# Kernel tuning notes

Hardware: AMD Instinct MI355X
Metric: run time of the kernel (lower is better)

## Reference

```python
import jax, jax.numpy as jnp
import numpy as np

N_NODES = 100000
N_EDGES = 1600000
F_IN = 500
HIDDEN = 64
N_CLASS = 40


def gcn_conv(x, W, b, src, dst, n_nodes):
    """PyG GCNConv: add self-loops, symmetric deg^-1/2 normalization,
    linear transform then scatter-add aggregation at dst."""
    h = x @ W  # [N, out]
    loop = jnp.arange(n_nodes, dtype=src.dtype)
    s = jnp.concatenate([src, loop])  # sources incl. self-loops
    d = jnp.concatenate([dst, loop])
    deg = jax.ops.segment_sum(jnp.ones_like(d, dtype=h.dtype), d, num_segments=n_nodes)
    dinv = jnp.where(deg > 0, jax.lax.rsqrt(deg), 0.0)
    norm = dinv[s] * dinv[d]  # [E+N]
    msg = h[s] * norm[:, None]  # gather + scale, [E+N, out]
    out = jax.ops.segment_sum(msg, d, num_segments=n_nodes)
    return out + b


def setup_inputs() -> dict:
    key = jax.random.key(0)
    k1, k2, k3, k4 = jax.random.split(key, 4)
    x = jax.random.normal(k1, (N_NODES, F_IN), dtype=jnp.float32)
    edge_index = jax.random.randint(k2, (2, N_EDGES), 0, N_NODES, dtype=jnp.int64)
    # Glorot-style init for GCNConv weights
    W1 = jax.random.normal(k3, (F_IN, HIDDEN), dtype=jnp.float32) / np.sqrt(F_IN)
    b1 = jnp.zeros((HIDDEN,), dtype=jnp.float32)
    W2 = jax.random.normal(k4, (HIDDEN, N_CLASS), dtype=jnp.float32) / np.sqrt(HIDDEN)
    b2 = jnp.zeros((N_CLASS,), dtype=jnp.float32)
    return {"x": x, "W1": W1, "b1": b1, "W2": W2, "b2": b2, "edge_index": edge_index}


def reference(x, W1, b1, W2, b2, edge_index):
    src, dst = edge_index[0], edge_index[1]
    n = x.shape[0]
    h = jax.nn.relu(gcn_conv(x, W1, b1, src, dst, n))
    # dropout is identity in eval mode (F.dropout with training=False)
    out = gcn_conv(h, W2, b2, src, dst, n)
    return jax.nn.log_softmax(out, axis=1)
```

## Files before the change

### kernel.cpp

```cpp
#include <hip/hip_runtime.h>
#include <math.h>

#define N_NODES 100000
#define N_EDGES 1600000
#define F_IN    500
#define HIDDEN  64
#define N_CLASS 40
#define KPAD    512

#define NB   2048
#define NPB  49
#define EPB  16384
#define CAP  1536

typedef __attribute__((ext_vector_type(4))) float f32x4;
typedef __attribute__((ext_vector_type(8))) __bf16 bf16x8;

__device__ __forceinline__ unsigned short f2bf(float f) {
    unsigned int u = __float_as_uint(f);
    u = (u + 0x7FFF + ((u >> 16) & 1)) >> 16;
    return (unsigned short)u;
}
__device__ __forceinline__ float bfu_lo(unsigned int v) {
    return __uint_as_float(v << 16);
}
__device__ __forceinline__ float bfu_hi(unsigned int v) {
    return __uint_as_float(v & 0xFFFF0000u);
}

__global__ void k_prep_w1t(const float* __restrict__ w1, unsigned short* __restrict__ w1t,
                           int* __restrict__ bcnt) {
    int idx = blockIdx.x * blockDim.x + threadIdx.x;
    if (idx < NB) bcnt[idx] = 0;
    if (idx >= HIDDEN * KPAD) return;
    int n = idx >> 9, k = idx & (KPAD - 1);
    float v = (k < F_IN) ? w1[k * HIDDEN + n] : 0.f;
    w1t[idx] = f2bf(v);
}

__launch_bounds__(1024)
__global__ void k_bhist(const int* __restrict__ dst, int* __restrict__ bcnt, int e) {
    __shared__ int h[NB];
    for (int i = threadIdx.x; i < NB; i += 1024) h[i] = 0;
    __syncthreads();
    int base = blockIdx.x * EPB;
#pragma unroll
    for (int j = 0; j < 16; ++j) {
        int i = base + j * 1024 + threadIdx.x;
        if (i < e) atomicAdd(&h[dst[i] / NPB], 1);
    }
    __syncthreads();
    for (int i = threadIdx.x; i < NB; i += 1024)
        if (h[i]) atomicAdd(&bcnt[i], h[i]);
}

__launch_bounds__(1024)
__global__ void k_bscan(const int* __restrict__ bcnt, int* __restrict__ bptr,
                        int* __restrict__ bcur) {
    __shared__ int s[1024];
    int t = threadIdx.x;
    int a = bcnt[2 * t], b = bcnt[2 * t + 1];
    int v = a + b;
    s[t] = v;
    __syncthreads();
    for (int off = 1; off < 1024; off <<= 1) {
        int u = (t >= off) ? s[t - off] : 0;
        __syncthreads();
        s[t] += u;
        __syncthreads();
    }
    int excl = s[t] - v;
    bptr[2 * t] = excl;     bptr[2 * t + 1] = excl + a;
    bcur[2 * t] = excl;     bcur[2 * t + 1] = excl + a;
    if (t == 1023) bptr[NB] = s[1023];
}

__launch_bounds__(1024)
__global__ void k_bfill(const int* __restrict__ src, const int* __restrict__ dst,
                        int* __restrict__ bcur, int2* __restrict__ ebuf, int e) {
    __shared__ int hist[NB];
    __shared__ int base_[NB];
    for (int i = threadIdx.x; i < NB; i += 1024) hist[i] = 0;
    __syncthreads();
    int b0 = blockIdx.x * EPB;
    int s_[16], d_[16];
#pragma unroll
    for (int j = 0; j < 16; ++j) {
        int i = b0 + j * 1024 + threadIdx.x;
        if (i < e) {
            s_[j] = src[i];
            d_[j] = dst[i];
            atomicAdd(&hist[d_[j] / NPB], 1);
        } else d_[j] = -1;
    }
    __syncthreads();
    for (int i = threadIdx.x; i < NB; i += 1024) {
        int hc = hist[i];
        base_[i] = hc ? atomicAdd(&bcur[i], hc) : 0;
        hist[i] = 0;
    }
    __syncthreads();
#pragma unroll
    for (int j = 0; j < 16; ++j) {
        if (d_[j] >= 0) {
            int bu = d_[j] / NPB;
            int r = atomicAdd(&hist[bu], 1);
            ebuf[base_[bu] + r] = make_int2(s_[j], d_[j]);
        }
    }
}

__launch_bounds__(256)
__global__ void k_bucket_csr(const int2* __restrict__ ebuf, const int* __restrict__ bptr,
                             int* __restrict__ rp, int* __restrict__ col,
                             float* __restrict__ dinv, int n) {
    int b  = blockIdx.x;
    int lo = b * NPB;
    if (lo >= n) return;
    int hi  = min(lo + NPB, n);
    int eb0 = bptr[b], ec = bptr[b + 1] - eb0;

    __shared__ int2 pairs[CAP];
    __shared__ int  hist[NPB];
    __shared__ int  excl[NPB + 1];
    for (int j = threadIdx.x; j < NPB; j += 256) hist[j] = 0;
    __syncthreads();
    for (int i = threadIdx.x; i < ec; i += 256) {
        int2 p = ebuf[eb0 + i];
        if (i < CAP) pairs[i] = p;
        atomicAdd(&hist[p.y - lo], 1);
    }
    __syncthreads();
    if (threadIdx.x == 0) {
        int acc = 0;
        for (int j = 0; j < NPB; ++j) { excl[j] = acc; acc += hist[j]; }
        excl[NPB] = acc;
    }
    __syncthreads();
    for (int j = threadIdx.x; j < hi - lo; j += 256) {
        rp[lo + j]   = eb0 + excl[j];
        dinv[lo + j] = rsqrtf((float)(hist[j] + 1));
    }
    if (hi == n && threadIdx.x == 0) rp[n] = eb0 + ec;
    __syncthreads();
    for (int j = threadIdx.x; j < NPB; j += 256) hist[j] = 0;
    __syncthreads();
    for (int i = threadIdx.x; i < ec; i += 256) {
        int2 p  = (i < CAP) ? pairs[i] : ebuf[eb0 + i];
        int  li = p.y - lo;
        int  r  = atomicAdd(&hist[li], 1);
        col[eb0 + excl[li] + r] = p.x;
    }
}

__launch_bounds__(256)
__global__ void k_gemm1(const float* __restrict__ x, const unsigned short* __restrict__ w1t,
                        const float* __restrict__ dinv, unsigned short* __restrict__ hs, int n) {
    __shared__ unsigned short xs[4][32][40];
    const int tid  = threadIdx.x;
    const int wave = tid >> 6;
    const int lane = tid & 63;
    const int quad = lane >> 4;
    const int l16  = lane & 15;
    const int rowb = blockIdx.x * 128 + wave * 32;

    const int srow = lane >> 3;
    const int skof = (lane & 7) * 4;

    f32x4 acc[2][4];
#pragma unroll
    for (int rt = 0; rt < 2; ++rt)
#pragma unroll
        for (int ct = 0; ct < 4; ++ct) acc[rt][ct] = (f32x4)0.f;

    for (int ks = 0; ks < 16; ++ks) {
        const int k0 = ks * 32;

        float4 tmp[4];
        if (ks < 15) {
#pragma unroll
            for (int u = 0; u < 4; ++u) {
                int grow = rowb + u * 8 + srow;
                tmp[u] = (grow < n) ? *(const float4*)&x[(size_t)grow * F_IN + k0 + skof]
                                    : make_float4(0.f, 0.f, 0.f, 0.f);
            }
        } else {
#pragma unroll
            for (int u = 0; u < 4; ++u) {
                int grow = rowb + u * 8 + srow;
                const float* p = &x[(size_t)grow * F_IN];
                float v0 = (grow < n && k0 + skof + 0 < F_IN) ? p[k0 + skof + 0] : 0.f;
                float v1 = (grow < n && k0 + skof + 1 < F_IN) ? p[k0 + skof + 1] : 0.f;
                float v2 = (grow < n && k0 + skof + 2 < F_IN) ? p[k0 + skof + 2] : 0.f;
                float v3 = (grow < n && k0 + skof + 3 < F_IN) ? p[k0 + skof + 3] : 0.f;
                tmp[u] = make_float4(v0, v1, v2, v3);
            }
        }
        bf16x8 bfrag[4];
#pragma unroll
        for (int ct = 0; ct < 4; ++ct)
            bfrag[ct] = *(const bf16x8*)&w1t[(ct * 16 + l16) * KPAD + k0 + quad * 8];

#pragma unroll
        for (int u = 0; u < 4; ++u) {
            unsigned int lo = (unsigned int)f2bf(tmp[u].x) | ((unsigned int)f2bf(tmp[u].y) << 16);
            unsigned int hi = (unsigned int)f2bf(tmp[u].z) | ((unsigned int)f2bf(tmp[u].w) << 16);
            *(uint2*)&xs[wave][u * 8 + srow][skof] = make_uint2(lo, hi);
        }
        __syncthreads();

        union { bf16x8 v; unsigned int u[4]; } af[2];
#pragma unroll
        for (int rt = 0; rt < 2; ++rt) {
            uint2 a = *(const uint2*)&xs[wave][rt * 16 + l16][quad * 8];
            uint2 b = *(const uint2*)&xs[wave][rt * 16 + l16][quad * 8 + 4];
            af[rt].u[0] = a.x; af[rt].u[1] = a.y; af[rt].u[2] = b.x; af[rt].u[3] = b.y;
        }
#pragma unroll
        for (int rt = 0; rt < 2; ++rt)
#pragma unroll
            for (int ct = 0; ct < 4; ++ct)
                acc[rt][ct] = __builtin_amdgcn_mfma_f32_16x16x32_bf16(
                    af[rt].v, bfrag[ct], acc[rt][ct], 0, 0, 0);
        __syncthreads();
    }

#pragma unroll
    for (int rt = 0; rt < 2; ++rt) {
#pragma unroll
        for (int reg = 0; reg < 4; ++reg) {
            int grow = rowb + rt * 16 + quad * 4 + reg;
            if (grow < n) {
                float dv = dinv[grow];
#pragma unroll
                for (int ct = 0; ct < 4; ++ct)
                    hs[(size_t)grow * HIDDEN + ct * 16 + l16] = f2bf(dv * acc[rt][ct][reg]);
            }
        }
    }
}

template <int F, bool RELU, bool LSM>
__launch_bounds__(256)
__global__ void k_agg(const uint2* __restrict__ hs2, const int* __restrict__ rp,
                      const int* __restrict__ col, const float* __restrict__ dinv,
                      const float* __restrict__ bias, float* __restrict__ out, int n) {
    constexpr int PW2 = F / 4;
    const int lane = threadIdx.x & 63;
    const int q    = lane >> 4;
    const int p    = lane & 15;
    const bool act = p < PW2;
    int wid = __builtin_amdgcn_readfirstlane((blockIdx.x * blockDim.x + threadIdx.x) >> 6);
    const int nw = (gridDim.x * blockDim.x) >> 6;

    for (; wid < n; wid += nw) {
        const int beg = rp[wid], end = rp[wid + 1];
        float a0 = 0.f, a1 = 0.f, a2 = 0.f, a3 = 0.f;
        int e = beg + q;
        for (; e + 12 < end; e += 16) {
            int c0 = col[e], c1 = col[e + 4], c2 = col[e + 8], c3 = col[e + 12];
            uint2 v0 = act ? hs2[(unsigned)c0 * PW2 + p] : make_uint2(0u, 0u);
            uint2 v1 = act ? hs2[(unsigned)c1 * PW2 + p] : make_uint2(0u, 0u);
            uint2 v2 = act ? hs2[(unsigned)c2 * PW2 + p] : make_uint2(0u, 0u);
            uint2 v3 = act ? hs2[(unsigned)c3 * PW2 + p] : make_uint2(0u, 0u);
            a0 += bfu_lo(v0.x) + bfu_lo(v1.x) + bfu_lo(v2.x) + bfu_lo(v3.x);
            a1 += bfu_hi(v0.x) + bfu_hi(v1.x) + bfu_hi(v2.x) + bfu_hi(v3.x);
            a2 += bfu_lo(v0.y) + bfu_lo(v1.y) + bfu_lo(v2.y) + bfu_lo(v3.y);
            a3 += bfu_hi(v0.y) + bfu_hi(v1.y) + bfu_hi(v2.y) + bfu_hi(v3.y);
        }
        if (e + 4 < end) {
            int c0 = col[e], c1 = col[e + 4];
            uint2 v0 = act ? hs2[(unsigned)c0 * PW2 + p] : make_uint2(0u, 0u);
            uint2 v1 = act ? hs2[(unsigned)c1 * PW2 + p] : make_uint2(0u, 0u);
            a0 += bfu_lo(v0.x) + bfu_lo(v1.x);
            a1 += bfu_hi(v0.x) + bfu_hi(v1.x);
            a2 += bfu_lo(v0.y) + bfu_lo(v1.y);
            a3 += bfu_hi(v0.y) + bfu_hi(v1.y);
            e += 8;
        }
        if (e < end) {
            int c0 = col[e];
            uint2 v0 = act ? hs2[(unsigned)c0 * PW2 + p] : make_uint2(0u, 0u);
            a0 += bfu_lo(v0.x); a1 += bfu_hi(v0.x);
            a2 += bfu_lo(v0.y); a3 += bfu_hi(v0.y);
        }
        a0 += __shfl_xor(a0, 16); a1 += __shfl_xor(a1, 16);
        a2 += __shfl_xor(a2, 16); a3 += __shfl_xor(a3, 16);
        a0 += __shfl_xor(a0, 32); a1 += __shfl_xor(a1, 32);
        a2 += __shfl_xor(a2, 32); a3 += __shfl_xor(a3, 32);

        const float di = dinv[wid];
        uint2 sv  = act ? hs2[(unsigned)wid * PW2 + p] : make_uint2(0u, 0u);
        float4 bv = act ? *(const float4*)&bias[4 * p] : make_float4(0.f, 0.f, 0.f, 0.f);
        float r0 = di * (a0 + bfu_lo(sv.x)) + bv.x;
        float r1 = di * (a1 + bfu_hi(sv.x)) + bv.y;
        float r2 = di * (a2 + bfu_lo(sv.y)) + bv.z;
        float r3 = di * (a3 + bfu_hi(sv.y)) + bv.w;
        if (RELU) {
            r0 = fmaxf(r0, 0.f); r1 = fmaxf(r1, 0.f);
            r2 = fmaxf(r2, 0.f); r3 = fmaxf(r3, 0.f);
        }
        if (LSM) {
            float m = act ? fmaxf(fmaxf(r0, r1), fmaxf(r2, r3)) : -INFINITY;
#pragma unroll
            for (int off = 8; off; off >>= 1) m = fmaxf(m, __shfl_xor(m, off));
            float ex = act ? (__expf(r0 - m) + __expf(r1 - m) + __expf(r2 - m) + __expf(r3 - m))
                           : 0.f;
#pragma unroll
            for (int off = 8; off; off >>= 1) ex += __shfl_xor(ex, off);
            float lse = m + __logf(ex);
            r0 -= lse; r1 -= lse; r2 -= lse; r3 -= lse;
        }
        if (q == 0 && act)
            *(float4*)&out[(size_t)wid * F + 4 * p] = make_float4(r0, r1, r2, r3);
    }
}

__launch_bounds__(256)
__global__ void k_gemm2(const float* __restrict__ a, const float* __restrict__ w,
                        const float* __restrict__ dinv, unsigned short* __restrict__ out, int n) {
    __shared__ float ws[HIDDEN * N_CLASS];
    for (int idx = threadIdx.x; idx < HIDDEN * N_CLASS; idx += 256) ws[idx] = w[idx];
    __syncthreads();
    int idx = blockIdx.x * 256 + threadIdx.x;
    if (idx >= n * N_CLASS) return;
    int i = idx / N_CLASS, j = idx - i * N_CLASS;
    float s = 0.f;
#pragma unroll
    for (int k = 0; k < HIDDEN; k += 4) {
        float4 xv = *(const float4*)&a[(size_t)i * HIDDEN + k];
        s = fmaf(xv.x, ws[k * N_CLASS + j], s);
        s = fmaf(xv.y, ws[(k + 1) * N_CLASS + j], s);
        s = fmaf(xv.z, ws[(k + 2) * N_CLASS + j], s);
        s = fmaf(xv.w, ws[(k + 3) * N_CLASS + j], s);
    }
    out[idx] = f2bf(dinv[i] * s);
}

extern "C" void kernel_launch(void* const* d_in, const int* in_sizes, int n_in,
                              void* d_out, int out_size, void* d_ws, size_t ws_size,
                              hipStream_t stream) {
    const float* x   = (const float*)d_in[0];
    const float* W1  = (const float*)d_in[1];
    const float* b1  = (const float*)d_in[2];
    const float* W2  = (const float*)d_in[3];
    const float* b2  = (const float*)d_in[4];
    const int*   ei  = (const int*)d_in[5];
    const int*   src = ei;
    const int*   dst = ei + N_EDGES;
    float*       out = (float*)d_out;

    char*  ws  = (char*)d_ws;
    size_t off = 0;
    auto alloc = [&](size_t bytes) -> void* {
        void* p = ws + off;
        off += (bytes + 255) & ~(size_t)255;
        return p;
    };
    int*            bcnt = (int*)alloc((size_t)NB * 4);
    int*            bptr = (int*)alloc((size_t)(NB + 1) * 4);
    int*            bcur = (int*)alloc((size_t)NB * 4);
    int*            rp   = (int*)alloc((size_t)(N_NODES + 1) * 4);
    int*            col  = (int*)alloc((size_t)N_EDGES * 4);
    float*          dinv = (float*)alloc((size_t)N_NODES * 4);
    unsigned short* w1t  = (unsigned short*)alloc((size_t)HIDDEN * KPAD * 2);
    unsigned short* h1s  = (unsigned short*)alloc((size_t)N_NODES * HIDDEN * 2);
    float*          h1a  = (float*)alloc((size_t)N_NODES * HIDDEN * 4);
    int2*           ebuf = (int2*)h1a;
    unsigned short* h2s  = h1s;

    const int NBH = (N_EDGES + EPB - 1) / EPB;

    k_prep_w1t<<<(HIDDEN * KPAD + 255) / 256, 256, 0, stream>>>(W1, w1t, bcnt);
    k_bhist<<<NBH, 1024, 0, stream>>>(dst, bcnt, N_EDGES);
    k_bscan<<<1, 1024, 0, stream>>>(bcnt, bptr, bcur);
    k_bfill<<<NBH, 1024, 0, stream>>>(src, dst, bcur, ebuf, N_EDGES);
    k_bucket_csr<<<NB, 256, 0, stream>>>(ebuf, bptr, rp, col, dinv, N_NODES);

    k_gemm1<<<(N_NODES + 127) / 128, 256, 0, stream>>>(x, w1t, dinv, h1s, N_NODES);
    k_agg<HIDDEN, true, false><<<2048, 256, 0, stream>>>(
        (const uint2*)h1s, rp, col, dinv, b1, h1a, N_NODES);

    k_gemm2<<<(N_NODES * N_CLASS + 255) / 256, 256, 0, stream>>>(h1a, W2, dinv, h2s, N_NODES);
    k_agg<N_CLASS, false, true><<<2048, 256, 0, stream>>>(
        (const uint2*)h2s, rp, col, dinv, b2, out, N_NODES);
}
```

Baseline: 497.7 us.

## Fuse second-layer GEMM into first aggregation and widen gather loads

The layer-1 aggregation now applies the 64x40 W2 transform in its epilogue. Each wave stages its finished row in LDS and writes the bf16 pre-scaled layer-2 features directly. This removes the fp32 hidden buffer round trip and the separate k_gemm2 launch. The aggregation kernel switches from 16 lanes x uint2 to 8 lanes x uint4 per row, so it issues fewer, wider gather loads. k_gemm1 gets a per-wave double-buffered LDS tile with register prefetch of the next K slice and drops its block barriers. This relies on each wave touching only its own LDS slice.

```diff
diff --git a/kernel.cpp b/kernel.cpp
--- a/kernel.cpp
+++ b/kernel.cpp
@@ -156,7 +156,7 @@
 __launch_bounds__(256)
 __global__ void k_gemm1(const float* __restrict__ x, const unsigned short* __restrict__ w1t,
                         const float* __restrict__ dinv, unsigned short* __restrict__ hs, int n) {
-    __shared__ unsigned short xs[4][32][40];
+    __shared__ __align__(16) unsigned short xs[4][2][32][40];
     const int tid  = threadIdx.x;
     const int wave = tid >> 6;
     const int lane = tid & 63;
@@ -173,16 +173,14 @@
 #pragma unroll
         for (int ct = 0; ct < 4; ++ct) acc[rt][ct] = (f32x4)0.f;
 
-    for (int ks = 0; ks < 16; ++ks) {
+    auto LOAD = [&](float4 (&t)[4], int ks) {
         const int k0 = ks * 32;
-
-        float4 tmp[4];
         if (ks < 15) {
 #pragma unroll
             for (int u = 0; u < 4; ++u) {
                 int grow = rowb + u * 8 + srow;
-                tmp[u] = (grow < n) ? *(const float4*)&x[(size_t)grow * F_IN + k0 + skof]
-                                    : make_float4(0.f, 0.f, 0.f, 0.f);
+                t[u] = (grow < n) ? *(const float4*)&x[(size_t)grow * F_IN + k0 + skof]
+                                  : make_float4(0.f, 0.f, 0.f, 0.f);
             }
         } else {
 #pragma unroll
@@ -193,36 +191,41 @@
                 float v1 = (grow < n && k0 + skof + 1 < F_IN) ? p[k0 + skof + 1] : 0.f;
                 float v2 = (grow < n && k0 + skof + 2 < F_IN) ? p[k0 + skof + 2] : 0.f;
                 float v3 = (grow < n && k0 + skof + 3 < F_IN) ? p[k0 + skof + 3] : 0.f;
-                tmp[u] = make_float4(v0, v1, v2, v3);
-            }
-        }
+                t[u] = make_float4(v0, v1, v2, v3);
+            }
+        }
+    };
+    auto STASH = [&](const float4 (&t)[4], int buf) {
+#pragma unroll
+        for (int u = 0; u < 4; ++u) {
+            unsigned int lo = (unsigned int)f2bf(t[u].x) | ((unsigned int)f2bf(t[u].y) << 16);
+            unsigned int hi = (unsigned int)f2bf(t[u].z) | ((unsigned int)f2bf(t[u].w) << 16);
+            *(uint2*)&xs[wave][buf][u * 8 + srow][skof] = make_uint2(lo, hi);
+        }
+    };
+
+    float4 tcur[4], tnx[4];
+    LOAD(tcur, 0);
+    STASH(tcur, 0);
+    for (int ks = 0; ks < 16; ++ks) {
+        const int buf = ks & 1;
+        if (ks < 15) LOAD(tnx, ks + 1);
+        const int k0 = ks * 32;
         bf16x8 bfrag[4];
 #pragma unroll
         for (int ct = 0; ct < 4; ++ct)
             bfrag[ct] = *(const bf16x8*)&w1t[(ct * 16 + l16) * KPAD + k0 + quad * 8];
-
-#pragma unroll
-        for (int u = 0; u < 4; ++u) {
-            unsigned int lo = (unsigned int)f2bf(tmp[u].x) | ((unsigned int)f2bf(tmp[u].y) << 16);
-            unsigned int hi = (unsigned int)f2bf(tmp[u].z) | ((unsigned int)f2bf(tmp[u].w) << 16);
-            *(uint2*)&xs[wave][u * 8 + srow][skof] = make_uint2(lo, hi);
-        }
-        __syncthreads();
-
-        union { bf16x8 v; unsigned int u[4]; } af[2];
-#pragma unroll
-        for (int rt = 0; rt < 2; ++rt) {
-            uint2 a = *(const uint2*)&xs[wave][rt * 16 + l16][quad * 8];
-            uint2 b = *(const uint2*)&xs[wave][rt * 16 + l16][quad * 8 + 4];
-            af[rt].u[0] = a.x; af[rt].u[1] = a.y; af[rt].u[2] = b.x; af[rt].u[3] = b.y;
-        }
+        bf16x8 af[2];
+#pragma unroll
+        for (int rt = 0; rt < 2; ++rt)
+            af[rt] = *(const bf16x8*)&xs[wave][buf][rt * 16 + l16][quad * 8];
 #pragma unroll
         for (int rt = 0; rt < 2; ++rt)
 #pragma unroll
             for (int ct = 0; ct < 4; ++ct)
                 acc[rt][ct] = __builtin_amdgcn_mfma_f32_16x16x32_bf16(
-                    af[rt].v, bfrag[ct], acc[rt][ct], 0, 0, 0);
-        __syncthreads();
+                    af[rt], bfrag[ct], acc[rt][ct], 0, 0, 0);
+        if (ks < 15) STASH(tnx, buf ^ 1);
     }
 
 #pragma unroll
@@ -240,101 +243,129 @@
     }
 }
 
-template <int F, bool RELU, bool LSM>
+template <int F, bool RELU, bool LSM, bool FUSE>
 __launch_bounds__(256)
-__global__ void k_agg(const uint2* __restrict__ hs2, const int* __restrict__ rp,
+__global__ void k_agg(const uint4* __restrict__ hs4, const int* __restrict__ rp,
                       const int* __restrict__ col, const float* __restrict__ dinv,
-                      const float* __restrict__ bias, float* __restrict__ out, int n) {
-    constexpr int PW2 = F / 4;
+                      const float* __restrict__ bias, float* __restrict__ outf,
+                      unsigned short* __restrict__ outh, const float* __restrict__ w2,
+                      int n) {
+    constexpr int PW4 = (F + 7) / 8;
+    __shared__ float ws2[FUSE ? HIDDEN * N_CLASS : 1];
+    __shared__ float rowbuf[FUSE ? 4 : 1][FUSE ? HIDDEN : 1];
+    if constexpr (FUSE) {
+        for (int i = threadIdx.x; i < HIDDEN * N_CLASS; i += 256) ws2[i] = w2[i];
+        __syncthreads();
+    }
     const int lane = threadIdx.x & 63;
-    const int q    = lane >> 4;
-    const int p    = lane & 15;
-    const bool act = p < PW2;
+    const int wave = threadIdx.x >> 6;
+    const int q    = lane >> 3;
+    const int p    = lane & 7;
+    const bool act = p < PW4;
     int wid = __builtin_amdgcn_readfirstlane((blockIdx.x * blockDim.x + threadIdx.x) >> 6);
     const int nw = (gridDim.x * blockDim.x) >> 6;
+    const uint4 z = make_uint4(0u, 0u, 0u, 0u);
 
     for (; wid < n; wid += nw) {
         const int beg = rp[wid], end = rp[wid + 1];
-        float a0 = 0.f, a1 = 0.f, a2 = 0.f, a3 = 0.f;
+        float a[8];
+#pragma unroll
+        for (int i = 0; i < 8; ++i) a[i] = 0.f;
+        auto ACC = [&](uint4 v) {
+            a[0] += bfu_lo(v.x); a[1] += bfu_hi(v.x);
+            a[2] += bfu_lo(v.y); a[3] += bfu_hi(v.y);
+            a[4] += bfu_lo(v.z); a[5] += bfu_hi(v.z);
+            a[6] += bfu_lo(v.w); a[7] += bfu_hi(v.w);
+        };
         int e = beg + q;
-        for (; e + 12 < end; e += 16) {
-            int c0 = col[e], c1 = col[e + 4], c2 = col[e + 8], c3 = col[e + 12];
-            uint2 v0 = act ? hs2[(unsigned)c0 * PW2 + p] : make_uint2(0u, 0u);
-            uint2 v1 = act ? hs2[(unsigned)c1 * PW2 + p] : make_uint2(0u, 0u);
-            uint2 v2 = act ? hs2[(unsigned)c2 * PW2 + p] : make_uint2(0u, 0u);
-            uint2 v3 = act ? hs2[(unsigned)c3 * PW2 + p] : make_uint2(0u, 0u);
-            a0 += bfu_lo(v0.x) + bfu_lo(v1.x) + bfu_lo(v2.x) + bfu_lo(v3.x);
-            a1 += bfu_hi(v0.x) + bfu_hi(v1.x) + bfu_hi(v2.x) + bfu_hi(v3.x);
-            a2 += bfu_lo(v0.y) + bfu_lo(v1.y) + bfu_lo(v2.y) + bfu_lo(v3.y);
-            a3 += bfu_hi(v0.y) + bfu_hi(v1.y) + bfu_hi(v2.y) + bfu_hi(v3.y);
-        }
-        if (e + 4 < end) {
-            int c0 = col[e], c1 = col[e + 4];
-            uint2 v0 = act ? hs2[(unsigned)c0 * PW2 + p] : make_uint2(0u, 0u);
-            uint2 v1 = act ? hs2[(unsigned)c1 * PW2 + p] : make_uint2(0u, 0u);
-            a0 += bfu_lo(v0.x) + bfu_lo(v1.x);
-            a1 += bfu_hi(v0.x) + bfu_hi(v1.x);
-            a2 += bfu_lo(v0.y) + bfu_lo(v1.y);
-            a3 += bfu_hi(v0.y) + bfu_hi(v1.y);
-            e += 8;
-        }
-        if (e < end) {
-            int c0 = col[e];
-            uint2 v0 = act ? hs2[(unsigned)c0 * PW2 + p] : make_uint2(0u, 0u);
-            a0 += bfu_lo(v0.x); a1 += bfu_hi(v0.x);
-            a2 += bfu_lo(v0.y); a3 += bfu_hi(v0.y);
-        }
-        a0 += __shfl_xor(a0, 16); a1 += __shfl_xor(a1, 16);
-        a2 += __shfl_xor(a2, 16); a3 += __shfl_xor(a3, 16);
-        a0 += __shfl_xor(a0, 32); a1 += __shfl_xor(a1, 32);
-        a2 += __shfl_xor(a2, 32); a3 += __shfl_xor(a3, 32);
+        for (; e + 24 < end; e += 32) {
+            int c0 = col[e], c1 = col[e + 8], c2 = col[e + 16], c3 = col[e + 24];
+            uint4 v0 = act ? hs4[(unsigned)c0 * PW4 + p] : z;
+            uint4 v1 = act ? hs4[(unsigned)c1 * PW4 + p] : z;
+            uint4 v2 = act ? hs4[(unsigned)c2 * PW4 + p] : z;
+            uint4 v3 = act ? hs4[(unsigned)c3 * PW4 + p] : z;
+            ACC(v0); ACC(v1); ACC(v2); ACC(v3);
+        }
+        {
+            const bool g0 = e < end, g1 = e + 8 < end, g2 = e + 16 < end;
+            int c0 = g0 ? col[e] : 0;
+            int c1 = g1 ? col[e + 8] : 0;
+            int c2 = g2 ? col[e + 16] : 0;
+            uint4 v0 = (act && g0) ? hs4[(unsigned)c0 * PW4 + p] : z;
+            uint4 v1 = (act && g1) ? hs4[(unsigned)c1 * PW4 + p] : z;
+            uint4 v2 = (act && g2) ? hs4[(unsigned)c2 * PW4 + p] : z;
+            ACC(v0); ACC(v1); ACC(v2);
+        }
+#pragma unroll
+        for (int i = 0; i < 8; ++i) {
+            a[i] += __shfl_xor(a[i], 8);
+            a[i] += __shfl_xor(a[i], 16);
+            a[i] += __shfl_xor(a[i], 32);
+        }
 
         const float di = dinv[wid];
-        uint2 sv  = act ? hs2[(unsigned)wid * PW2 + p] : make_uint2(0u, 0u);
-        float4 bv = act ? *(const float4*)&bias[4 * p] : make_float4(0.f, 0.f, 0.f, 0.f);
-        float r0 = di * (a0 + bfu_lo(sv.x)) + bv.x;
-        float r1 = di * (a1 + bfu_hi(sv.x)) + bv.y;
-        float r2 = di * (a2 + bfu_lo(sv.y)) + bv.z;
-        float r3 = di * (a3 + bfu_hi(sv.y)) + bv.w;
-        if (RELU) {
-            r0 = fmaxf(r0, 0.f); r1 = fmaxf(r1, 0.f);
-            r2 = fmaxf(r2, 0.f); r3 = fmaxf(r3, 0.f);
-        }
-        if (LSM) {
-            float m = act ? fmaxf(fmaxf(r0, r1), fmaxf(r2, r3)) : -INFINITY;
-#pragma unroll
-            for (int off = 8; off; off >>= 1) m = fmaxf(m, __shfl_xor(m, off));
-            float ex = act ? (__expf(r0 - m) + __expf(r1 - m) + __expf(r2 - m) + __expf(r3 - m))
-                           : 0.f;
-#pragma unroll
-            for (int off = 8; off; off >>= 1) ex += __shfl_xor(ex, off);
+        uint4 sv = act ? hs4[(unsigned)wid * PW4 + p] : z;
+        float s[8] = {bfu_lo(sv.x), bfu_hi(sv.x), bfu_lo(sv.y), bfu_hi(sv.y),
+                      bfu_lo(sv.z), bfu_hi(sv.z), bfu_lo(sv.w), bfu_hi(sv.w)};
+        float bv[8];
+        if (act) {
+            float4 t0 = *(const float4*)&bias[8 * p];
+            float4 t1 = *(const float4*)&bias[8 * p + 4];
+            bv[0] = t0.x; bv[1] = t0.y; bv[2] = t0.z; bv[3] = t0.w;
+            bv[4] = t1.x; bv[5] = t1.y; bv[6] = t1.z; bv[7] = t1.w;
+        } else {
+#pragma unroll
+            for (int i = 0; i < 8; ++i) bv[i] = 0.f;
+        }
+        float r[8];
+#pragma unroll
+        for (int i = 0; i < 8; ++i) {
+            r[i] = di * (a[i] + s[i]) + bv[i];
+            if (RELU) r[i] = fmaxf(r[i], 0.f);
+        }
+        if constexpr (LSM) {
+            float m = -INFINITY;
+            if (act) {
+#pragma unroll
+                for (int i = 0; i < 8; ++i) m = fmaxf(m, r[i]);
+            }
+#pragma unroll
+            for (int off = 4; off; off >>= 1) m = fmaxf(m, __shfl_xor(m, off));
+            float ex = 0.f;
+            if (act) {
+#pragma unroll
+                for (int i = 0; i < 8; ++i) ex += __expf(r[i] - m);
+            }
+#pragma unroll
+            for (int off = 4; off; off >>= 1) ex += __shfl_xor(ex, off);
             float lse = m + __logf(ex);
-            r0 -= lse; r1 -= lse; r2 -= lse; r3 -= lse;
-        }
-        if (q == 0 && act)
-            *(float4*)&out[(size_t)wid * F + 4 * p] = make_float4(r0, r1, r2, r3);
-    }
-}
-
-__launch_bounds__(256)
-__global__ void k_gemm2(const float* __restrict__ a, const float* __restrict__ w,
-                        const float* __restrict__ dinv, unsigned short* __restrict__ out, int n) {
-    __shared__ float ws[HIDDEN * N_CLASS];
-    for (int idx = threadIdx.x; idx < HIDDEN * N_CLASS; idx += 256) ws[idx] = w[idx];
-    __syncthreads();
-    int idx = blockIdx.x * 256 + threadIdx.x;
-    if (idx >= n * N_CLASS) return;
-    int i = idx / N_CLASS, j = idx - i * N_CLASS;
-    float s = 0.f;
-#pragma unroll
-    for (int k = 0; k < HIDDEN; k += 4) {
-        float4 xv = *(const float4*)&a[(size_t)i * HIDDEN + k];
-        s = fmaf(xv.x, ws[k * N_CLASS + j], s);
-        s = fmaf(xv.y, ws[(k + 1) * N_CLASS + j], s);
-        s = fmaf(xv.z, ws[(k + 2) * N_CLASS + j], s);
-        s = fmaf(xv.w, ws[(k + 3) * N_CLASS + j], s);
-    }
-    out[idx] = f2bf(dinv[i] * s);
+#pragma unroll
+            for (int i = 0; i < 8; ++i) r[i] -= lse;
+        }
+        if constexpr (FUSE) {
+            if (q == 0 && act) {
+                *(float4*)&rowbuf[wave][8 * p]     = make_float4(r[0], r[1], r[2], r[3]);
+                *(float4*)&rowbuf[wave][8 * p + 4] = make_float4(r[4], r[5], r[6], r[7]);
+            }
+            if (lane < N_CLASS) {
+                float y = 0.f;
+#pragma unroll
+                for (int k = 0; k < HIDDEN; k += 4) {
+                    float4 rv = *(const float4*)&rowbuf[wave][k];
+                    y = fmaf(rv.x, ws2[(k + 0) * N_CLASS + lane], y);
+                    y = fmaf(rv.y, ws2[(k + 1) * N_CLASS + lane], y);
+                    y = fmaf(rv.z, ws2[(k + 2) * N_CLASS + lane], y);
+                    y = fmaf(rv.w, ws2[(k + 3) * N_CLASS + lane], y);
+                }
+                outh[(size_t)wid * N_CLASS + lane] = f2bf(di * y);
+            }
+        } else {
+            if (q == 0 && act) {
+                *(float4*)&outf[(size_t)wid * F + 8 * p]     = make_float4(r[0], r[1], r[2], r[3]);
+                *(float4*)&outf[(size_t)wid * F + 8 * p + 4] = make_float4(r[4], r[5], r[6], r[7]);
+            }
+        }
+    }
 }
 
 extern "C" void kernel_launch(void* const* d_in, const int* in_sizes, int n_in,
@@ -365,9 +396,8 @@
     float*          dinv = (float*)alloc((size_t)N_NODES * 4);
     unsigned short* w1t  = (unsigned short*)alloc((size_t)HIDDEN * KPAD * 2);
     unsigned short* h1s  = (unsigned short*)alloc((size_t)N_NODES * HIDDEN * 2);
-    float*          h1a  = (float*)alloc((size_t)N_NODES * HIDDEN * 4);
-    int2*           ebuf = (int2*)h1a;
-    unsigned short* h2s  = h1s;
+    int2*           ebuf = (int2*)alloc((size_t)N_EDGES * 8);
+    unsigned short* h2s  = (unsigned short*)ebuf;
 
     const int NBH = (N_EDGES + EPB - 1) / EPB;
 
@@ -378,10 +408,9 @@
     k_bucket_csr<<<NB, 256, 0, stream>>>(ebuf, bptr, rp, col, dinv, N_NODES);
 
     k_gemm1<<<(N_NODES + 127) / 128, 256, 0, stream>>>(x, w1t, dinv, h1s, N_NODES);
-    k_agg<HIDDEN, true, false><<<2048, 256, 0, stream>>>(
-        (const uint2*)h1s, rp, col, dinv, b1, h1a, N_NODES);
-
-    k_gemm2<<<(N_NODES * N_CLASS + 255) / 256, 256, 0, stream>>>(h1a, W2, dinv, h2s, N_NODES);
-    k_agg<N_CLASS, false, true><<<2048, 256, 0, stream>>>(
-        (const uint2*)h2s, rp, col, dinv, b2, out, N_NODES);
-}
+    k_agg<HIDDEN, true, false, true><<<2048, 256, 0, stream>>>(
+        (const uint4*)h1s, rp, col, dinv, b1, nullptr, h2s, W2, N_NODES);
+
+    k_agg<N_CLASS, false, true, false><<<2048, 256, 0, stream>>>(
+        (const uint4*)h2s, rp, col, dinv, b2, out, nullptr, nullptr, N_NODES);
+}
```

After: 535.0 us. 1.07x slower.
